# Kernel tuning notes

Measured on AMD Instinct MI355X. Metric: run time of the kernel, lower is better.

Reference implementation:

```python
import jax, jax.numpy as jnp
import numpy as np

B, S, D = 2, 2048, 2048
VOCAB = 32000
CUTOFFS = [1000, 2000, 5000, VOCAB]  # torch appends vocab_size
N_CLUSTERS = 3
HEAD_SIZE = CUTOFFS[0] + N_CLUSTERS  # 1003
LN_EPS = 1e-5
INIT = 0.02


def setup_inputs() -> dict:
    key = jax.random.key(0)
    ks = jax.random.split(key, 10)
    inp = {
        "x": jax.random.normal(ks[0], (B, S, D), dtype=jnp.float32),
        "targets": jax.random.randint(ks[1], (B, S), 0, VOCAB, dtype=jnp.int32),
        "gamma": jnp.ones((D,), jnp.float32),
        "beta": jnp.zeros((D,), jnp.float32),
        "head_w": jax.random.normal(ks[2], (HEAD_SIZE, D), jnp.float32) * INIT,
    }
    # tail clusters: hsz = D // 4**i, osz = cutoffs[i] - cutoffs[i-1]
    for i in range(1, 4):
        hsz = D // (4 ** i)
        osz = CUTOFFS[i] - CUTOFFS[i - 1]
        inp[f"t{i}_w1"] = jax.random.normal(ks[2 + 2 * i], (hsz, D), jnp.float32) * INIT
        inp[f"t{i}_w2"] = jax.random.normal(ks[3 + 2 * i], (osz, hsz), jnp.float32) * INIT
    return inp


def reference(x, targets, gamma, beta, head_w, t1_w1, t1_w2, t2_w1, t2_w2, t3_w1, t3_w2):
    # LayerNorm over last dim
    mu = jnp.mean(x, axis=-1, keepdims=True)
    var = jnp.mean(jnp.square(x - mu), axis=-1, keepdims=True)
    xn = (x - mu) * jax.lax.rsqrt(var + LN_EPS) * gamma + beta

    # shift: predict token t+1 from hidden t
    h = xn[:, :-1, :].reshape(-1, x.shape[-1])      # [N, D]
    lbl = targets[:, 1:].reshape(-1)                # [N]
    n = h.shape[0]
    rows = jnp.arange(n)

    # head: shortlist (first cutoff) + one logit per tail cluster
    head_lp = jax.nn.log_softmax(h @ head_w.T, axis=-1)  # [N, 1003]
    out = head_lp[rows, jnp.clip(lbl, 0, CUTOFFS[0] - 1)]

    tails = [(t1_w1, t1_w2), (t2_w1, t2_w2), (t3_w1, t3_w2)]
    for i, (w1, w2) in enumerate(tails):
        low, high = CUTOFFS[i], CUTOFFS[i + 1]
        tail_lp = jax.nn.log_softmax((h @ w1.T) @ w2.T, axis=-1)  # [N, osz]
        rel = jnp.clip(lbl - low, 0, high - low - 1)
        lp = head_lp[:, CUTOFFS[0] + i] + tail_lp[rows, rel]
        out = jnp.where((lbl >= low) & (lbl < high), lp, out)

    return -jnp.mean(out)  # NLL loss, matches .loss of AdaptiveLogSoftmaxWithLoss
```

## Files before the change

### kernel.cpp

```cpp
#include <hip/hip_runtime.h>
#include <hip/hip_bf16.h>
#include <math.h>

#define BB 2
#define SS 2048
#define DD 2048
#define NR (BB*(SS-1))
#define NRP 4096
#define MT_LD 768
#define MT_P2 512
#define MT_P3 640

#define L2E 1.4426950408889634f
#define LN2F 0.6931471805599453f
#define LSE_SHIFT 4.0f
#define LSE_NC (-LSE_SHIFT * L2E)
#define WSCALE 16.0f
#define WINV   0.0625f

typedef short  bh8   __attribute__((ext_vector_type(8)));
typedef float  f32x4 __attribute__((ext_vector_type(4)));
typedef long   l64x2 __attribute__((ext_vector_type(2)));

__device__ inline float bfl(unsigned short b) { return __uint_as_float(((unsigned)b) << 16); }
__device__ inline float expsh(float v) { return __builtin_amdgcn_exp2f(fmaf(v, L2E, LSE_NC)); }

__device__ inline float block_sum256(float v) {
    __shared__ float tmp[4];
    #pragma unroll
    for (int o = 32; o > 0; o >>= 1) v += __shfl_down(v, o, 64);
    int lane = threadIdx.x & 63, w = threadIdx.x >> 6;
    if (lane == 0) tmp[w] = v;
    __syncthreads();
    float r = tmp[0] + tmp[1] + tmp[2] + tmp[3];
    __syncthreads();
    return r;
}

__device__ inline unsigned pack_fp8x4(float a, float b, float c, float d) {
    unsigned r = 0;
    r = __builtin_amdgcn_cvt_pk_fp8_f32(a, b, r, false);
    r = __builtin_amdgcn_cvt_pk_fp8_f32(c, d, r, true);
    return r;
}

struct CastSegs {
    const float* src[7];
    void* dst[7];
    int n_src[7];
    int n_tot[7];
    int b0[7];
    int isfp8[7];
    float scl[7];
};
struct AParams {
    const float* x; const float* gamma; const float* beta;
    unsigned char* h8;
    CastSegs sg; int castBlocks;
    const int* targets;
    int *relH, *rel1, *rel2, *rel3;
    float *S0, *S1, *S2, *out;
};

__global__ __launch_bounds__(256) void stageA(AParams p) {
    int blk = blockIdx.x, tid = threadIdx.x;
    if (blk < NRP) {
        int n = blk;
        unsigned char* hr = p.h8 + (size_t)n * DD;
        if (n >= NR) { *(uint2*)(hr + tid * 8) = make_uint2(0,0); return; }
        int b = n / (SS - 1), t = n % (SS - 1);
        const float4* xr = (const float4*)(p.x + (size_t)(b * SS + t) * DD);
        float4 a = xr[tid * 2];
        float4 c = xr[tid * 2 + 1];
        float sum = a.x + a.y + a.z + a.w + c.x + c.y + c.z + c.w;
        sum = block_sum256(sum);
        float mu = sum * (1.0f / DD);
        float d[8] = {a.x-mu, a.y-mu, a.z-mu, a.w-mu, c.x-mu, c.y-mu, c.z-mu, c.w-mu};
        float sq = 0.f;
        #pragma unroll
        for (int i = 0; i < 8; ++i) sq += d[i] * d[i];
        sq = block_sum256(sq);
        float rstd = rsqrtf(sq * (1.0f / DD) + 1e-5f);
        const float4* g4 = (const float4*)p.gamma;
        const float4* be4 = (const float4*)p.beta;
        float4 g1 = g4[tid*2], g2 = g4[tid*2+1];
        float4 b1 = be4[tid*2], b2 = be4[tid*2+1];
        float gg[8] = {g1.x,g1.y,g1.z,g1.w,g2.x,g2.y,g2.z,g2.w};
        float bb[8] = {b1.x,b1.y,b1.z,b1.w,b2.x,b2.y,b2.z,b2.w};
        float o[8];
        #pragma unroll
        for (int i = 0; i < 8; ++i) o[i] = d[i] * rstd * gg[i] + bb[i];
        uint2 pk;
        pk.x = pack_fp8x4(o[0], o[1], o[2], o[3]);
        pk.y = pack_fp8x4(o[4], o[5], o[6], o[7]);
        *(uint2*)(hr + tid * 8) = pk;
        return;
    }
    blk -= NRP;
    if (blk < p.castBlocks) {
        int k = 0;
        #pragma unroll
        for (int i = 1; i < 7; ++i) if (blk >= p.sg.b0[i]) k = i;
        int i4 = (blk - p.sg.b0[k]) * 1024 + tid * 4;
        if (i4 >= p.sg.n_tot[k]) return;
        float4 v = make_float4(0.f,0.f,0.f,0.f);
        if (i4 < p.sg.n_src[k]) v = *(const float4*)(p.sg.src[k] + i4);
        if (p.sg.isfp8[k]) {
            unsigned pk = pack_fp8x4(v.x * WSCALE, v.y * WSCALE, v.z * WSCALE, v.w * WSCALE);
            *(unsigned*)((unsigned char*)p.sg.dst[k] + i4) = pk;
        } else {
            float sc = p.sg.scl[k];
            __align__(8) __hip_bfloat16 o[4] = {
                __float2bfloat16(v.x * sc), __float2bfloat16(v.y * sc),
                __float2bfloat16(v.z * sc), __float2bfloat16(v.w * sc)};
            *(uint2*)((__hip_bfloat16*)p.sg.dst[k] + i4) = *(uint2*)o;
        }
        return;
    }
    blk -= p.castBlocks;
    int n = blk * 256 + tid;
    if (n >= NRP) return;
    int lbl = -1;
    if (n < NR) {
        int b = n / (SS - 1), t = n % (SS - 1);
        lbl = p.targets[b * SS + t + 1];
    }
    bool v = n < NR;
    p.relH[n] = v ? (lbl < 1000 ? lbl : 999) : -1;
    int r1 = lbl - 1000;  p.rel1[n] = v ? (r1 < 0 ? 0 : (r1 > 999   ? 999   : r1)) : -1;
    int r2 = lbl - 2000;  p.rel2[n] = v ? (r2 < 0 ? 0 : (r2 > 2999  ? 2999  : r2)) : -1;
    int r3 = lbl - 5000;  p.rel3[n] = v ? (r3 < 0 ? 0 : (r3 > 26999 ? 26999 : r3)) : -1;
    p.S0[n] = 0.f; p.S1[n] = 0.f; p.S2[n] = 0.f;
    if (n == 0) p.out[0] = 0.f;
}

__global__ __launch_bounds__(256) void megaF(
        const unsigned char* __restrict__ A,
        const unsigned char* __restrict__ W,
        __hip_bfloat16* __restrict__ megaT,
        const int* __restrict__ relH,
        float* __restrict__ S0, float* __restrict__ aux) {
    __shared__ __align__(16) unsigned char smF[2][16384];
    int tid = threadIdx.x, wv = tid >> 6, lane = tid & 63;
    int row0 = blockIdx.y * 128, col0 = blockIdx.x * 128;
    int wrow = (wv >> 1) * 64, wcol = (wv & 1) * 64;
    f32x4 acc[4][4];
    #pragma unroll
    for (int i = 0; i < 4; ++i)
        #pragma unroll
        for (int j = 0; j < 4; ++j) acc[i][j] = (f32x4){0.f,0.f,0.f,0.f};
    int sr = lane >> 2;
    int kp = (lane & 3) * 16;
    int mrow = lane & 15;
    int q16 = (lane >> 4) * 16;

    auto stage = [&](int buf, int k0) {
        #pragma unroll
        for (int i = 0; i < 2; ++i) {
            int chunk = wv * 2 + i;
            int r = chunk * 16 + sr;
            const void* ga = A + (size_t)(row0 + r) * DD + k0 + kp;
            const void* gw = W + (size_t)(col0 + r) * DD + k0 + kp;
            void* la = (char*)&smF[buf][0]    + chunk * 1024 + lane * 16;
            void* lw = (char*)&smF[buf][8192] + chunk * 1024 + lane * 16;
            __builtin_amdgcn_global_load_lds(
                (const __attribute__((address_space(1))) void*)ga,
                (__attribute__((address_space(3))) void*)la, 16, 0, 0);
            __builtin_amdgcn_global_load_lds(
                (const __attribute__((address_space(1))) void*)gw,
                (__attribute__((address_space(3))) void*)lw, 16, 0, 0);
        }
    };

    stage(0, 0);
    asm volatile("s_waitcnt vmcnt(0)" ::: "memory");
    __builtin_amdgcn_s_barrier();
    __builtin_amdgcn_sched_barrier(0);
    int cur = 0;
    for (int k0 = 0; k0 < DD; k0 += 64) {
        if (k0 + 64 < DD) stage(cur ^ 1, k0 + 64);
        const unsigned char* As = &smF[cur][0];
        const unsigned char* Ws = &smF[cur][8192];
        l64x2 af[4], bfr[4];
        #pragma unroll
        for (int t = 0; t < 4; ++t) {
            af[t]  = *(const l64x2*)(As + (wrow + t*16 + mrow) * 64 + q16);
            bfr[t] = *(const l64x2*)(Ws + (wcol + t*16 + mrow) * 64 + q16);
        }
        #pragma unroll
        for (int s = 0; s < 2; ++s)
            #pragma unroll
            for (int i = 0; i < 4; ++i)
                #pragma unroll
                for (int j = 0; j < 4; ++j)
                    acc[i][j] = __builtin_amdgcn_mfma_f32_16x16x32_fp8_fp8(
                        af[i][s], bfr[j][s], acc[i][j], 0, 0, 0);
        asm volatile("s_waitcnt vmcnt(0) lgkmcnt(0)" ::: "memory");
        __builtin_amdgcn_s_barrier();
        __builtin_amdgcn_sched_barrier(0);
        cur ^= 1;
    }
    int ccol = lane & 15, g = lane >> 4;
    if (blockIdx.x < 8) {
        int grs[4][4], rh[4][4];
        float ps[4][4];
        #pragma unroll
        for (int i = 0; i < 4; ++i)
            #pragma unroll
            for (int r = 0; r < 4; ++r) {
                grs[i][r] = row0 + wrow + i*16 + g*4 + r;
                rh[i][r] = relH[grs[i][r]];
                ps[i][r] = 0.f;
            }
        #pragma unroll
        for (int i = 0; i < 4; ++i)
            #pragma unroll
            for (int j = 0; j < 4; ++j) {
                int gc = col0 + wcol + j*16 + ccol;
                bool inr = gc < 1003;
                #pragma unroll
                for (int r = 0; r < 4; ++r) {
                    float v = acc[i][j][r] * WINV;
                    if (gc == rh[i][r]) aux[grs[i][r]*8 + 0] = v;
                    if (gc >= 1000 && gc < 1003) aux[grs[i][r]*8 + 2 + (gc - 1000)] = v;
                    ps[i][r] += inr ? expsh(v) : 0.f;
                }
            }
        #pragma unroll
        for (int off = 1; off < 16; off <<= 1)
            #pragma unroll
            for (int i = 0; i < 4; ++i)
                #pragma unroll
                for (int r = 0; r < 4; ++r) ps[i][r] += __shfl_xor(ps[i][r], off, 64);
        if (ccol == 0)
            #pragma unroll
            for (int i = 0; i < 4; ++i)
                #pragma unroll
                for (int r = 0; r < 4; ++r) atomicAdd(&S0[grs[i][r]], ps[i][r]);
    } else {
        int cb = col0 - 1024 + wcol;
        #pragma unroll
        for (int i = 0; i < 4; ++i) {
            size_t gr0 = row0 + wrow + i*16 + g*4;
            #pragma unroll
            for (int j = 0; j < 4; ++j) {
                size_t gc = cb + j*16 + ccol;
                #pragma unroll
                for (int r = 0; r < 4; ++r)
                    megaT[(gr0 + r) * MT_LD + gc] = __float2bfloat16(acc[i][j][r] * WINV);
            }
        }
    }
}

__device__ void tail_gemm(const __hip_bfloat16* A, int lda,
        const __hip_bfloat16* W, int K, int bx, int by, int validCols,
        const int* rel, float* S, float* tgt, char* sm) {
    int tid = threadIdx.x, wv = tid >> 6, lane = tid & 63;
    int row0 = by * 64, col0 = bx * 128;
    int wrow = (wv >> 1) * 32, wcol = (wv & 1) * 64;
    f32x4 acc[2][4];
    #pragma unroll
    for (int i = 0; i < 2; ++i)
        #pragma unroll
        for (int j = 0; j < 4; ++j) acc[i][j] = (f32x4){0.f,0.f,0.f,0.f};
    int sr = lane >> 2, sk = (lane & 3) * 8, mrow = lane & 15, q16 = (lane >> 4) * 16;
    int nt = K >> 5;

    auto stage = [&](int buf, int k0) {
        char* base = sm + buf * 12288;
        #pragma unroll
        for (int i = 0; i < 3; ++i) {
            int c = wv * 3 + i;
            const __hip_bfloat16* gsrc;
            char* ldst;
            if (c < 4) {
                gsrc = A + (size_t)(row0 + c * 16 + sr) * lda + k0 + sk;
                ldst = base + c * 1024 + lane * 16;
            } else {
                int cw = c - 4;
                gsrc = W + (size_t)(col0 + cw * 16 + sr) * K + k0 + sk;
                ldst = base + 4096 + cw * 1024 + lane * 16;
            }
            __builtin_amdgcn_global_load_lds(
                (const __attribute__((address_space(1))) void*)gsrc,
                (__attribute__((address_space(3))) void*)ldst, 16, 0, 0);
        }
    };

    stage(0, 0);
    asm volatile("s_waitcnt vmcnt(0)" ::: "memory");
    __builtin_amdgcn_s_barrier();
    __builtin_amdgcn_sched_barrier(0);
    int cur = 0;
    for (int t = 0; t < nt; ++t) {
        if (t + 1 < nt) stage(cur ^ 1, (t + 1) << 5);
        const char* As = sm + cur * 12288;
        const char* Ws = As + 4096;
        bh8 af[2], bfr[4];
        #pragma unroll
        for (int u = 0; u < 2; ++u)
            af[u] = *(const bh8*)(As + (wrow + u*16 + mrow) * 64 + q16);
        #pragma unroll
        for (int u = 0; u < 4; ++u)
            bfr[u] = *(const bh8*)(Ws + (wcol + u*16 + mrow) * 64 + q16);
        #pragma unroll
        for (int i = 0; i < 2; ++i)
            #pragma unroll
            for (int j = 0; j < 4; ++j)
                acc[i][j] = __builtin_amdgcn_mfma_f32_16x16x32_bf16(af[i], bfr[j], acc[i][j], 0, 0, 0);
        asm volatile("s_waitcnt vmcnt(0) lgkmcnt(0)" ::: "memory");
        __builtin_amdgcn_s_barrier();
        __builtin_amdgcn_sched_barrier(0);
        cur ^= 1;
    }
    int ccol = lane & 15, g = lane >> 4;
    int grs[2][4], rh[2][4];
    float p[2][4];
    #pragma unroll
    for (int i = 0; i < 2; ++i)
        #pragma unroll
        for (int r = 0; r < 4; ++r) {
            grs[i][r] = row0 + wrow + i*16 + g*4 + r;
            rh[i][r] = rel[grs[i][r]];
            p[i][r] = 0.f;
        }
    #pragma unroll
    for (int i = 0; i < 2; ++i)
        #pragma unroll
        for (int j = 0; j < 4; ++j) {
            int gc = col0 + wcol + j*16 + ccol;
            bool inr = gc < validCols;
            #pragma unroll
            for (int r = 0; r < 4; ++r) {
                float v = acc[i][j][r];
                if (gc == rh[i][r]) tgt[grs[i][r]] = v;
                p[i][r] += inr ? expsh(v) : 0.f;
            }
        }
    #pragma unroll
    for (int off = 1; off < 16; off <<= 1)
        #pragma unroll
        for (int i = 0; i < 2; ++i)
            #pragma unroll
            for (int r = 0; r < 4; ++r) p[i][r] += __shfl_xor(p[i][r], off, 64);
    if (ccol == 0)
        #pragma unroll
        for (int i = 0; i < 2; ++i)
            #pragma unroll
            for (int r = 0; r < 4; ++r) atomicAdd(&S[grs[i][r]], p[i][r]);
}

#define T3_TILES 1688
#define T3_SPLIT 16
#define T3_TPC   106
__device__ void t3_partial_body(const __hip_bfloat16* megaT,
        const __hip_bfloat16* w2b, float* pS, int idx, int tid, float* red ) {
    int rg = idx >> 4, cs = idx & 15;
    int wv = tid >> 6, lane = tid & 63;
    int q = lane >> 4, cm = lane & 15;
    int row0 = rg * 64;
    bh8 af[4];
    #pragma unroll
    for (int h = 0; h < 4; ++h)
        af[h] = *(const bh8*)(megaT + (size_t)(row0 + h*16 + cm) * MT_LD + MT_P3 + q * 8);
    int tile0 = cs * T3_TPC;
    int tile1 = tile0 + T3_TPC; if (tile1 > T3_TILES) tile1 = T3_TILES;
    float s[4][4];
    #pragma unroll
    for (int h = 0; h < 4; ++h)
        #pragma unroll
        for (int r = 0; r < 4; ++r) s[h][r] = 0.f;
    int ot = tile0 + wv;
    int oc0 = ot < tile1 ? ot : tile1 - 1;
    int oc1 = ot + 4 < tile1 ? ot + 4 : tile1 - 1;
    bh8 b0 = *(const bh8*)(w2b + (size_t)(oc0 * 16 + cm) * 32 + q * 8);
    bh8 b1 = *(const bh8*)(w2b + (size_t)(oc1 * 16 + cm) * 32 + q * 8);
    for (; ot < tile1; ot += 4) {
        bh8 bcur = b0;
        b0 = b1;
        int otn = ot + 8;
        if (otn < tile1)
            b1 = *(const bh8*)(w2b + (size_t)(otn * 16 + cm) * 32 + q * 8);
        f32x4 c[4];
        #pragma unroll
        for (int h = 0; h < 4; ++h)
            c[h] = __builtin_amdgcn_mfma_f32_16x16x32_bf16(af[h], bcur, (f32x4){0,0,0,0}, 0, 0, 0);
        #pragma unroll
        for (int h = 0; h < 4; ++h)
            #pragma unroll
            for (int r = 0; r < 4; ++r) s[h][r] += __builtin_amdgcn_exp2f(c[h][r]);
    }
    #pragma unroll
    for (int off = 1; off < 16; off <<= 1)
        #pragma unroll
        for (int h = 0; h < 4; ++h)
            #pragma unroll
            for (int r = 0; r < 4; ++r) s[h][r] += __shfl_xor(s[h][r], off, 64);
    if (cm == 0)
        #pragma unroll
        for (int h = 0; h < 4; ++h)
            #pragma unroll
            for (int r = 0; r < 4; ++r)
                red[wv * 64 + h*16 + q*4 + r] = s[h][r];
    __syncthreads();
    if (tid < 64)
        pS[(size_t)(row0 + tid) * 16 + cs] = red[tid] + red[64 + tid] + red[128 + tid] + red[192 + tid];
}

__device__ void t3_gather_body(const __hip_bfloat16* megaT, const __hip_bfloat16* w2b,
        const int* rel3, float* tt2, int idx, int tid) {
    int n = idx * 256 + tid;
    if (n >= NR) return;
    int rc = rel3[n];
    const unsigned short* pa = (const unsigned short*)(megaT + (size_t)n * MT_LD + MT_P3);
    const unsigned short* pw = (const unsigned short*)(w2b + (size_t)rc * 32);
    float acc = 0.f;
    #pragma unroll
    for (int k = 0; k < 32; ++k) acc += bfl(pa[k]) * bfl(pw[k]);
    tt2[n] = acc;
}

#define NT3 1024
#define NT1 512
#define NT2 1536
__global__ __launch_bounds__(256) void fatC(const __hip_bfloat16* __restrict__ megaT,
        const __hip_bfloat16* __restrict__ t1w2b, const __hip_bfloat16* __restrict__ t2w2b,
        const __hip_bfloat16* __restrict__ w2b3,
        const int* __restrict__ rel1, const int* __restrict__ rel2, const int* __restrict__ rel3,
        float* __restrict__ S1, float* __restrict__ S2, float* __restrict__ pS3,
        float* __restrict__ tt0, float* __restrict__ tt1, float* __restrict__ tt2) {
    __shared__ __align__(16) char sm[24576];
    int idx = blockIdx.x, tid = threadIdx.x;
    if (idx < NT3) { t3_partial_body(megaT, w2b3, pS3, idx, tid, (float*)sm); return; }
    idx -= NT3;
    if (idx < NT1) { tail_gemm(megaT, MT_LD, t1w2b, 512, idx % 8, idx / 8, 1000, rel1, S1, tt0, sm); return; }
    idx -= NT1;
    if (idx < NT2) { tail_gemm(megaT + MT_P2, MT_LD, t2w2b, 128, idx % 24, idx / 24, 3000, rel2, S2, tt1, sm); return; }
    idx -= NT2;
    t3_gather_body(megaT, w2b3, rel3, tt2, idx, tid);
}

__global__ __launch_bounds__(256) void final_kernel(const float* __restrict__ aux,
        const int* __restrict__ targets,
        const float* __restrict__ S0, const float* __restrict__ S1, const float* __restrict__ S2,
        const float* __restrict__ pS3,
        const float* __restrict__ tt0, const float* __restrict__ tt1, const float* __restrict__ tt2,
        float* __restrict__ out) {
    int n = blockIdx.x * 256 + threadIdx.x;
    float local = 0.f;
    if (n < NR) {
        int b = n / (SS - 1), t = n % (SS - 1);
        int lbl = targets[b * SS + t + 1];
        float lse = logf(S0[n]) + LSE_SHIFT;
        float o;
        if (lbl < 1000)      o = aux[n*8 + 0] - lse;
        else if (lbl < 2000) o = (aux[n*8 + 2] - lse) + (tt0[n] - (logf(S1[n]) + LSE_SHIFT));
        else if (lbl < 5000) o = (aux[n*8 + 3] - lse) + (tt1[n] - (logf(S2[n]) + LSE_SHIFT));
        else {
            float S3 = 0.f;
            #pragma unroll
            for (int c = 0; c < 16; ++c) S3 += pS3[n*16 + c];
            S3 -= 8.0f;
            o = (aux[n*8 + 4] - lse) + (tt2[n] * LN2F - logf(S3));
        }
        local = o;
    }
    local = block_sum256(local);
    if (threadIdx.x == 0) atomicAdd(out, -local / (float)NR);
}

extern "C" void kernel_launch(void* const* d_in, const int* in_sizes, int n_in,
                              void* d_out, int out_size, void* d_ws, size_t ws_size,
                              hipStream_t stream) {
    const float* x      = (const float*)d_in[0];
    const int*   targets= (const int*)d_in[1];
    const float* gamma  = (const float*)d_in[2];
    const float* beta   = (const float*)d_in[3];
    const float* head_w = (const float*)d_in[4];
    const float* t1_w1  = (const float*)d_in[5];
    const float* t1_w2  = (const float*)d_in[6];
    const float* t2_w1  = (const float*)d_in[7];
    const float* t2_w2  = (const float*)d_in[8];
    const float* t3_w1  = (const float*)d_in[9];
    const float* t3_w2  = (const float*)d_in[10];
    (void)in_sizes; (void)n_in; (void)out_size; (void)ws_size;

    char* base = (char*)d_ws;
    size_t off = 0;
    auto ab = [&](size_t nbytes) { char* p = base + off; off += (nbytes + 15) & ~(size_t)15; return p; };
    unsigned char* h8     = (unsigned char*)ab((size_t)NRP * DD);
    unsigned char* w1cat8 = (unsigned char*)ab((size_t)1792 * DD);
    __hip_bfloat16* megaT = (__hip_bfloat16*)ab((size_t)NRP * MT_LD * 2);
    __hip_bfloat16* t1w2b = (__hip_bfloat16*)ab((size_t)1024 * 512 * 2);
    __hip_bfloat16* t2w2b = (__hip_bfloat16*)ab((size_t)3072 * 128 * 2);
    __hip_bfloat16* w2b3  = (__hip_bfloat16*)ab((size_t)27008 * 32 * 2);
    float* aux = (float*)ab((size_t)NRP * 8 * 4);
    float* pS3 = (float*)ab((size_t)NRP * 16 * 4);
    float* S0  = (float*)ab(NRP * 4);
    float* S1  = (float*)ab(NRP * 4);
    float* S2  = (float*)ab(NRP * 4);
    int* relH  = (int*)ab(NRP * 4);
    int* rel1  = (int*)ab(NRP * 4);
    int* rel2  = (int*)ab(NRP * 4);
    int* rel3  = (int*)ab(NRP * 4);
    float* tt0 = (float*)ab(NRP * 4);
    float* tt1 = (float*)ab(NRP * 4);
    float* tt2 = (float*)ab(NRP * 4);

    AParams p;
    p.x = x; p.gamma = gamma; p.beta = beta; p.h8 = h8;
    p.targets = targets;
    p.relH = relH; p.rel1 = rel1; p.rel2 = rel2; p.rel3 = rel3;
    p.S0 = S0; p.S1 = S1; p.S2 = S2; p.out = (float*)d_out;
    const float* srcs[7] = {head_w, t1_w1, t2_w1, t3_w1, t1_w2, t2_w2, t3_w2};
    void* dsts[7] = {w1cat8, w1cat8 + (size_t)1024*2048, w1cat8 + (size_t)1536*2048,
                     w1cat8 + (size_t)1664*2048, t1w2b, t2w2b, w2b3};
    int nsrc[7] = {1003*2048, 512*2048, 128*2048, 32*2048, 1000*512, 3000*128, 27000*32};
    int ntot[7] = {1024*2048, 512*2048, 128*2048, 128*2048, 1024*512, 3072*128, 27008*32};
    int isf8[7] = {1, 1, 1, 1, 0, 0, 0};
    float scls[7] = {1.f, 1.f, 1.f, 1.f, 1.0f, 1.0f, L2E};
    int blk = 0;
    for (int i = 0; i < 7; ++i) {
        p.sg.src[i] = srcs[i]; p.sg.dst[i] = dsts[i];
        p.sg.n_src[i] = nsrc[i]; p.sg.n_tot[i] = ntot[i];
        p.sg.isfp8[i] = isf8[i];
        p.sg.scl[i] = scls[i];
        p.sg.b0[i] = blk;
        blk += (ntot[i] + 1023) / 1024;
    }
    p.castBlocks = blk;

    stageA<<<NRP + blk + 16, 256, 0, stream>>>(p);
    megaF<<<dim3(14, 32), 256, 0, stream>>>(h8, w1cat8, megaT, relH, S0, aux);
    fatC<<<NT3 + NT1 + NT2 + 16, 256, 0, stream>>>(megaT, t1w2b, t2w2b, w2b3,
            rel1, rel2, rel3, S1, S2, pS3, tt0, tt1, tt2);
    final_kernel<<<16, 256, 0, stream>>>(aux, targets, S0, S1, S2, pS3, tt0, tt1, tt2, (float*)d_out);
}
```

Before: 190.9 us.

## Swizzle LDS layouts, split tail kernel, widen T3 split and deepen prefetch

Adds an XOR swizzle to the LDS staging and read addresses in both the fp8 head GEMM and the bf16 tail GEMM to reduce bank conflicts. The tail GEMM drops double buffering for a single buffer with two syncthreads per step, which shrinks LDS use but exposes load latency. The fused tail kernel is split into separate T3 and T1/T2 launches. The T3 column split goes from 16 to 32 for more blocks, with the W2 register prefetch depth raised from 2 to 4 and a float4 reduction in the final kernel. The extra launch and the lost double buffering may offset the gains.

```diff
diff --git a/kernel.cpp b/kernel.cpp
--- a/kernel.cpp
+++ b/kernel.cpp
@@ -150,9 +150,9 @@
         #pragma unroll
         for (int j = 0; j < 4; ++j) acc[i][j] = (f32x4){0.f,0.f,0.f,0.f};
     int sr = lane >> 2;
-    int kp = (lane & 3) * 16;
+    int kp = (((lane & 3) ^ (sr & 3)) * 16);
     int mrow = lane & 15;
-    int q16 = (lane >> 4) * 16;
+    int qx = (((lane >> 4) ^ (lane & 3)) * 16);
 
     auto stage = [&](int buf, int k0) {
         #pragma unroll
@@ -184,8 +184,8 @@
         l64x2 af[4], bfr[4];
         #pragma unroll
         for (int t = 0; t < 4; ++t) {
-            af[t]  = *(const l64x2*)(As + (wrow + t*16 + mrow) * 64 + q16);
-            bfr[t] = *(const l64x2*)(Ws + (wcol + t*16 + mrow) * 64 + q16);
+            af[t]  = *(const l64x2*)(As + (wrow + t*16 + mrow) * 64 + qx);
+            bfr[t] = *(const l64x2*)(Ws + (wcol + t*16 + mrow) * 64 + qx);
         }
         #pragma unroll
         for (int s = 0; s < 2; ++s)
@@ -256,6 +256,8 @@
 __device__ void tail_gemm(const __hip_bfloat16* A, int lda,
         const __hip_bfloat16* W, int K, int bx, int by, int validCols,
         const int* rel, float* S, float* tgt, char* sm) {
+    __hip_bfloat16* As = (__hip_bfloat16*)sm;
+    __hip_bfloat16* Ws = (__hip_bfloat16*)(sm + 4096);
     int tid = threadIdx.x, wv = tid >> 6, lane = tid & 63;
     int row0 = by * 64, col0 = bx * 128;
     int wrow = (wv >> 1) * 32, wcol = (wv & 1) * 64;
@@ -264,11 +266,13 @@
     for (int i = 0; i < 2; ++i)
         #pragma unroll
         for (int j = 0; j < 4; ++j) acc[i][j] = (f32x4){0.f,0.f,0.f,0.f};
-    int sr = lane >> 2, sk = (lane & 3) * 8, mrow = lane & 15, q16 = (lane >> 4) * 16;
-    int nt = K >> 5;
-
-    auto stage = [&](int buf, int k0) {
-        char* base = sm + buf * 12288;
+    int sr = lane >> 2;
+    int sk = (((lane & 3) ^ (sr & 3)) * 8);
+    int mrow = lane & 15;
+    int qx = (((lane >> 4) ^ (lane & 3)) * 16);
+
+    for (int k0 = 0; k0 < K; k0 += 32) {
+        __syncthreads();
         #pragma unroll
         for (int i = 0; i < 3; ++i) {
             int c = wv * 3 + i;
@@ -276,43 +280,29 @@
             char* ldst;
             if (c < 4) {
                 gsrc = A + (size_t)(row0 + c * 16 + sr) * lda + k0 + sk;
-                ldst = base + c * 1024 + lane * 16;
+                ldst = (char*)As + c * 1024 + lane * 16;
             } else {
                 int cw = c - 4;
                 gsrc = W + (size_t)(col0 + cw * 16 + sr) * K + k0 + sk;
-                ldst = base + 4096 + cw * 1024 + lane * 16;
+                ldst = (char*)Ws + cw * 1024 + lane * 16;
             }
             __builtin_amdgcn_global_load_lds(
                 (const __attribute__((address_space(1))) void*)gsrc,
                 (__attribute__((address_space(3))) void*)ldst, 16, 0, 0);
         }
-    };
-
-    stage(0, 0);
-    asm volatile("s_waitcnt vmcnt(0)" ::: "memory");
-    __builtin_amdgcn_s_barrier();
-    __builtin_amdgcn_sched_barrier(0);
-    int cur = 0;
-    for (int t = 0; t < nt; ++t) {
-        if (t + 1 < nt) stage(cur ^ 1, (t + 1) << 5);
-        const char* As = sm + cur * 12288;
-        const char* Ws = As + 4096;
+        __syncthreads();
         bh8 af[2], bfr[4];
         #pragma unroll
-        for (int u = 0; u < 2; ++u)
-            af[u] = *(const bh8*)(As + (wrow + u*16 + mrow) * 64 + q16);
-        #pragma unroll
-        for (int u = 0; u < 4; ++u)
-            bfr[u] = *(const bh8*)(Ws + (wcol + u*16 + mrow) * 64 + q16);
+        for (int t = 0; t < 2; ++t)
+            af[t] = *(const bh8*)((const char*)As + (wrow + t*16 + mrow) * 64 + qx);
+        #pragma unroll
+        for (int t = 0; t < 4; ++t)
+            bfr[t] = *(const bh8*)((const char*)Ws + (wcol + t*16 + mrow) * 64 + qx);
         #pragma unroll
         for (int i = 0; i < 2; ++i)
             #pragma unroll
             for (int j = 0; j < 4; ++j)
                 acc[i][j] = __builtin_amdgcn_mfma_f32_16x16x32_bf16(af[i], bfr[j], acc[i][j], 0, 0, 0);
-        asm volatile("s_waitcnt vmcnt(0) lgkmcnt(0)" ::: "memory");
-        __builtin_amdgcn_s_barrier();
-        __builtin_amdgcn_sched_barrier(0);
-        cur ^= 1;
     }
     int ccol = lane & 15, g = lane >> 4;
     int grs[2][4], rh[2][4];
@@ -352,11 +342,11 @@
 }
 
 #define T3_TILES 1688
-#define T3_SPLIT 16
-#define T3_TPC   106
+#define T3_SPLIT 32
+#define T3_TPC   53
 __device__ void t3_partial_body(const __hip_bfloat16* megaT,
         const __hip_bfloat16* w2b, float* pS, int idx, int tid, float* red ) {
-    int rg = idx >> 4, cs = idx & 15;
+    int rg = idx >> 5, cs = idx & 31;
     int wv = tid >> 6, lane = tid & 63;
     int q = lane >> 4, cm = lane & 15;
     int row0 = rg * 64;
@@ -372,16 +362,17 @@
         #pragma unroll
         for (int r = 0; r < 4; ++r) s[h][r] = 0.f;
     int ot = tile0 + wv;
-    int oc0 = ot < tile1 ? ot : tile1 - 1;
-    int oc1 = ot + 4 < tile1 ? ot + 4 : tile1 - 1;
-    bh8 b0 = *(const bh8*)(w2b + (size_t)(oc0 * 16 + cm) * 32 + q * 8);
-    bh8 b1 = *(const bh8*)(w2b + (size_t)(oc1 * 16 + cm) * 32 + q * 8);
+    auto baddr = [&](int t) {
+        int tc = t < tile1 ? t : tile1 - 1;
+        return (const bh8*)(w2b + (size_t)(tc * 16 + cm) * 32 + q * 8);
+    };
+    bh8 p0 = *baddr(ot), p1 = *baddr(ot + 4), p2 = *baddr(ot + 8), p3 = *baddr(ot + 12);
     for (; ot < tile1; ot += 4) {
-        bh8 bcur = b0;
-        b0 = b1;
-        int otn = ot + 8;
+        bh8 bcur = p0;
+        p0 = p1; p1 = p2; p2 = p3;
+        int otn = ot + 16;
         if (otn < tile1)
-            b1 = *(const bh8*)(w2b + (size_t)(otn * 16 + cm) * 32 + q * 8);
+            p3 = *(const bh8*)(w2b + (size_t)(otn * 16 + cm) * 32 + q * 8);
         f32x4 c[4];
         #pragma unroll
         for (int h = 0; h < 4; ++h)
@@ -405,7 +396,8 @@
                 red[wv * 64 + h*16 + q*4 + r] = s[h][r];
     __syncthreads();
     if (tid < 64)
-        pS[(size_t)(row0 + tid) * 16 + cs] = red[tid] + red[64 + tid] + red[128 + tid] + red[192 + tid];
+        pS[(size_t)(row0 + tid) * T3_SPLIT + cs] =
+            red[tid] + red[64 + tid] + red[128 + tid] + red[192 + tid];
 }
 
 __device__ void t3_gather_body(const __hip_bfloat16* megaT, const __hip_bfloat16* w2b,
@@ -421,24 +413,29 @@
     tt2[n] = acc;
 }
 
-#define NT3 1024
+#define NT3 (64 * T3_SPLIT)
+__global__ __launch_bounds__(256) void fatT3(const __hip_bfloat16* __restrict__ megaT,
+        const __hip_bfloat16* __restrict__ w2b3, const int* __restrict__ rel3,
+        float* __restrict__ pS3, float* __restrict__ tt2) {
+    __shared__ __align__(16) float red[256];
+    int idx = blockIdx.x, tid = threadIdx.x;
+    if (idx < NT3) { t3_partial_body(megaT, w2b3, pS3, idx, tid, red); return; }
+    t3_gather_body(megaT, w2b3, rel3, tt2, idx - NT3, tid);
+}
+
 #define NT1 512
 #define NT2 1536
-__global__ __launch_bounds__(256) void fatC(const __hip_bfloat16* __restrict__ megaT,
+__global__ __launch_bounds__(256) void fatT12(const __hip_bfloat16* __restrict__ megaT,
         const __hip_bfloat16* __restrict__ t1w2b, const __hip_bfloat16* __restrict__ t2w2b,
-        const __hip_bfloat16* __restrict__ w2b3,
-        const int* __restrict__ rel1, const int* __restrict__ rel2, const int* __restrict__ rel3,
-        float* __restrict__ S1, float* __restrict__ S2, float* __restrict__ pS3,
-        float* __restrict__ tt0, float* __restrict__ tt1, float* __restrict__ tt2) {
-    __shared__ __align__(16) char sm[24576];
+        const int* __restrict__ rel1, const int* __restrict__ rel2,
+        float* __restrict__ S1, float* __restrict__ S2,
+        float* __restrict__ tt0, float* __restrict__ tt1) {
+    __shared__ __align__(16) char sm[12288];
     int idx = blockIdx.x, tid = threadIdx.x;
-    if (idx < NT3) { t3_partial_body(megaT, w2b3, pS3, idx, tid, (float*)sm); return; }
-    idx -= NT3;
     if (idx < NT1) { tail_gemm(megaT, MT_LD, t1w2b, 512, idx % 8, idx / 8, 1000, rel1, S1, tt0, sm); return; }
     idx -= NT1;
-    if (idx < NT2) { tail_gemm(megaT + MT_P2, MT_LD, t2w2b, 128, idx % 24, idx / 24, 3000, rel2, S2, tt1, sm); return; }
-    idx -= NT2;
-    t3_gather_body(megaT, w2b3, rel3, tt2, idx, tid);
+    tail_gemm(megaT + MT_P2, MT_LD, t2w2b, 128, idx % 24, idx / 24, 3000, rel2, S2, tt1, sm);
+    (void)tid;
 }
 
 __global__ __launch_bounds__(256) void final_kernel(const float* __restrict__ aux,
@@ -459,8 +456,12 @@
         else if (lbl < 5000) o = (aux[n*8 + 3] - lse) + (tt1[n] - (logf(S2[n]) + LSE_SHIFT));
         else {
             float S3 = 0.f;
-            #pragma unroll
-            for (int c = 0; c < 16; ++c) S3 += pS3[n*16 + c];
+            const float4* p4 = (const float4*)(pS3 + (size_t)n * T3_SPLIT);
+            #pragma unroll
+            for (int c = 0; c < T3_SPLIT/4; ++c) {
+                float4 v = p4[c];
+                S3 += v.x + v.y + v.z + v.w;
+            }
             S3 -= 8.0f;
             o = (aux[n*8 + 4] - lse) + (tt2[n] * LN2F - logf(S3));
         }
@@ -496,7 +497,7 @@
     __hip_bfloat16* t2w2b = (__hip_bfloat16*)ab((size_t)3072 * 128 * 2);
     __hip_bfloat16* w2b3  = (__hip_bfloat16*)ab((size_t)27008 * 32 * 2);
     float* aux = (float*)ab((size_t)NRP * 8 * 4);
-    float* pS3 = (float*)ab((size_t)NRP * 16 * 4);
+    float* pS3 = (float*)ab((size_t)NRP * T3_SPLIT * 4);
     float* S0  = (float*)ab(NRP * 4);
     float* S1  = (float*)ab(NRP * 4);
     float* S2  = (float*)ab(NRP * 4);
@@ -533,7 +534,7 @@
 
     stageA<<<NRP + blk + 16, 256, 0, stream>>>(p);
     megaF<<<dim3(14, 32), 256, 0, stream>>>(h8, w1cat8, megaT, relH, S0, aux);
-    fatC<<<NT3 + NT1 + NT2 + 16, 256, 0, stream>>>(megaT, t1w2b, t2w2b, w2b3,
-            rel1, rel2, rel3, S1, S2, pS3, tt0, tt1, tt2);
+    fatT3<<<NT3 + 16, 256, 0, stream>>>(megaT, w2b3, rel3, pS3, tt2);
+    fatT12<<<NT1 + NT2, 256, 0, stream>>>(megaT, t1w2b, t2w2b, rel1, rel2, S1, S2, tt0, tt1);
     final_kernel<<<16, 256, 0, stream>>>(aux, targets, S0, S1, S2, pS3, tt0, tt1, tt2, (float*)d_out);
 }
```

New measurement: 194.9 us. +2.1%, slower.
